# Kernel tuning notes

Measured on AMD Instinct MI355X. Metric: run time of the kernel, lower is better.

Reference implementation:

```python
import jax, jax.numpy as jnp
import numpy as np

TOP_K = 2


def setup_inputs() -> dict:
    key = jax.random.key(0)
    ks = jax.random.split(key, 5)
    B, N, C, FF, E = 2, 2048, 1024, 4096, 8
    x = jax.random.normal(ks[0], (B, N, C), dtype=jnp.float32)
    router_w = jax.random.normal(ks[1], (E, C), dtype=jnp.float32) * 0.02
    # xavier-uniform-like init for expert weights
    lim1 = np.sqrt(6.0 / (FF + C))
    expert_w1 = jax.random.uniform(ks[2], (E, FF, C), dtype=jnp.float32, minval=-lim1, maxval=lim1)
    expert_b1 = jnp.zeros((E, FF), dtype=jnp.float32)
    expert_w2 = jax.random.uniform(ks[3], (E, C, FF), dtype=jnp.float32, minval=-lim1, maxval=lim1)
    expert_b2 = jnp.zeros((E, C), dtype=jnp.float32)
    return {"x": x, "router_w": router_w, "expert_w1": expert_w1,
            "expert_b1": expert_b1, "expert_w2": expert_w2, "expert_b2": expert_b2}


def reference(x, router_w, expert_w1, expert_b1, expert_w2, expert_b2):
    # x: [B,N,C]; router_w: [E,C]; expert_w1: [E,FF,C]; expert_w2: [E,C,FF]
    router_logits = jnp.einsum('bnc,ec->bne', x, router_w)          # [B,N,E]
    router_probs = jax.nn.softmax(router_logits, axis=-1)
    expert_weights, expert_idx = jax.lax.top_k(router_probs, TOP_K)  # [B,N,K]
    expert_weights = expert_weights / (expert_weights.sum(axis=-1, keepdims=True) + 1e-9)
    # Dense all-expert FFN (avoids materializing per-token gathered weight matrices)
    h = jnp.einsum('bnc,efc->bnef', x, expert_w1) + expert_b1        # [B,N,E,FF]
    h = jax.nn.gelu(h, approximate=False)                            # torch nn.GELU = exact
    out_all = jnp.einsum('bnef,ecf->bnec', h, expert_w2) + expert_b2  # [B,N,E,C]
    # Gather top-k expert outputs and combine
    out_k = jnp.take_along_axis(out_all, expert_idx[..., None], axis=2)  # [B,N,K,C]
    return (out_k * expert_weights[..., None]).sum(axis=2)           # [B,N,C]
```

## Files before the change

### kernel.cpp

```cpp
#include <hip/hip_runtime.h>
#include <hip/hip_bf16.h>

#define TTOK  4096
#define CDIM  1024
#define FFDIM 4096
#define NEXP  8


typedef short short8 __attribute__((ext_vector_type(8)));
typedef float f32x4 __attribute__((ext_vector_type(4)));

__device__ __forceinline__ unsigned short f2bf(float f) {
    unsigned int u = __float_as_uint(f);
    u = u + 0x7fffu + ((u >> 16) & 1u);
    return (unsigned short)(u >> 16);
}

__global__ void cast_x_kernel(const float* __restrict__ x, unsigned short* __restrict__ xb) {
    int i = blockIdx.x * blockDim.x + threadIdx.x;
    float4 v = reinterpret_cast<const float4*>(x)[i];
    ushort4 o;
    o.x = f2bf(v.x); o.y = f2bf(v.y); o.z = f2bf(v.z); o.w = f2bf(v.w);
    reinterpret_cast<ushort4*>(xb)[i] = o;
}

__global__ void router_kernel(const float* __restrict__ x, const float* __restrict__ rw,
                              int* __restrict__ counts, int* __restrict__ btok,
                              float* __restrict__ bgate) {
    const int wave = threadIdx.x >> 6;
    const int lane = threadIdx.x & 63;
    const int t = blockIdx.x * 4 + wave;
    const float* xr = x + (size_t)t * CDIM;

    float acc[NEXP];
#pragma unroll
    for (int e = 0; e < NEXP; e++) acc[e] = 0.f;
    for (int c = lane; c < CDIM; c += 64) {
        float xv = xr[c];
#pragma unroll
        for (int e = 0; e < NEXP; e++) acc[e] += xv * rw[e * CDIM + c];
    }
#pragma unroll
    for (int e = 0; e < NEXP; e++) {
#pragma unroll
        for (int off = 32; off > 0; off >>= 1) acc[e] += __shfl_down(acc[e], off, 64);
    }
    if (lane == 0) {
        float mx = acc[0];
#pragma unroll
        for (int e = 1; e < NEXP; e++) mx = fmaxf(mx, acc[e]);
        float p[NEXP]; float s = 0.f;
#pragma unroll
        for (int e = 0; e < NEXP; e++) { p[e] = expf(acc[e] - mx); s += p[e]; }
        int i0 = 0;
#pragma unroll
        for (int e = 1; e < NEXP; e++) if (p[e] > p[i0]) i0 = e;
        int i1 = (i0 == 0) ? 1 : 0;
#pragma unroll
        for (int e = 0; e < NEXP; e++) if (e != i0 && p[e] > p[i1]) i1 = e;
        float pr0 = p[i0] / s, pr1 = p[i1] / s;
        float rs = 1.f / (pr0 + pr1 + 1e-9f);
        float w0 = pr0 * rs, w1 = pr1 * rs;
        int pos = atomicAdd(&counts[i0], 1);
        btok[i0 * TTOK + pos] = t; bgate[i0 * TTOK + pos] = w0;
        pos = atomicAdd(&counts[i1], 1);
        btok[i1 * TTOK + pos] = t; bgate[i1 * TTOK + pos] = w1;
    }
}

__global__ void offsets_kernel(const int* __restrict__ counts, int* __restrict__ offsets) {
    if (threadIdx.x == 0 && blockIdx.x == 0) {
        int s = 0;
        for (int e = 0; e < NEXP; e++) { offsets[e] = s; s += counts[e]; }
        offsets[NEXP] = s;
    }
}

__global__ __launch_bounds__(256) void gemm1_kernel(
    const unsigned short* __restrict__ xb, const float* __restrict__ w1,
    const float* __restrict__ b1, const int* __restrict__ counts,
    const int* __restrict__ offsets, const int* __restrict__ btok,
    unsigned short* __restrict__ H) {
    const int e = blockIdx.z;
    const int cnt = counts[e];
    const int m0 = blockIdx.y * 128;
    if (m0 >= cnt) return;
    const int n0 = blockIdx.x * 128;
    const int po = offsets[e];

    __shared__ unsigned short As[128][32];
    __shared__ unsigned short Bs[128][32];

    const int tid = threadIdx.x;
    const int wave = tid >> 6, lane = tid & 63;
    const int wm = (wave >> 1) << 6, wn = (wave & 1) << 6;
    const int lm = lane & 15, kq = lane >> 4;

    f32x4 acc[4][4];
#pragma unroll
    for (int i = 0; i < 4; i++)
#pragma unroll
        for (int j = 0; j < 4; j++) { f32x4 z = {0.f, 0.f, 0.f, 0.f}; acc[i][j] = z; }

    const float* w1e = w1 + (size_t)e * FFDIM * CDIM;
    const int arow = tid >> 1;
    const int acolb = (tid & 1) * 16;
    int tokA = -1;
    if (m0 + arow < cnt) tokA = btok[e * TTOK + m0 + arow];
    const int brow = tid >> 1;
    const int bcol = (tid & 1) * 16;

    for (int k0 = 0; k0 < CDIM; k0 += 32) {
        uint4 a0 = {0, 0, 0, 0}, a1 = {0, 0, 0, 0};
        if (tokA >= 0) {
            const uint4* src = reinterpret_cast<const uint4*>(xb + (size_t)tokA * CDIM + k0 + acolb);
            a0 = src[0]; a1 = src[1];
        }
        *reinterpret_cast<uint4*>(&As[arow][acolb]) = a0;
        *reinterpret_cast<uint4*>(&As[arow][acolb + 8]) = a1;
        {
            const float* src = w1e + (size_t)(n0 + brow) * CDIM + k0 + bcol;
            ushort4* dst = reinterpret_cast<ushort4*>(&Bs[brow][bcol]);
#pragma unroll
            for (int q = 0; q < 4; q++) {
                float4 v = reinterpret_cast<const float4*>(src)[q];
                ushort4 o; o.x = f2bf(v.x); o.y = f2bf(v.y); o.z = f2bf(v.z); o.w = f2bf(v.w);
                dst[q] = o;
            }
        }
        __syncthreads();
        short8 af[4], bfr[4];
#pragma unroll
        for (int i = 0; i < 4; i++) af[i] = *reinterpret_cast<const short8*>(&As[wm + i * 16 + lm][kq * 8]);
#pragma unroll
        for (int j = 0; j < 4; j++) bfr[j] = *reinterpret_cast<const short8*>(&Bs[wn + j * 16 + lm][kq * 8]);
#pragma unroll
        for (int i = 0; i < 4; i++)
#pragma unroll
            for (int j = 0; j < 4; j++)
                acc[i][j] = __builtin_amdgcn_mfma_f32_16x16x32_bf16(af[i], bfr[j], acc[i][j], 0, 0, 0);
        __syncthreads();
    }

#pragma unroll
    for (int j = 0; j < 4; j++) {
        const int fcol = n0 + wn + j * 16 + lm;
        const float bias = b1[e * FFDIM + fcol];
#pragma unroll
        for (int i = 0; i < 4; i++) {
#pragma unroll
            for (int r = 0; r < 4; r++) {
                const int mrow = m0 + wm + i * 16 + kq * 4 + r;
                if (mrow < cnt) {
                    float h = acc[i][j][r] + bias;
                    float g = 0.5f * h * (1.f + erff(h * 0.70710678118654752f));
                    H[(size_t)(po + mrow) * FFDIM + fcol] = f2bf(g);
                }
            }
        }
    }
}

__global__ __launch_bounds__(256) void gemm2_kernel(
    const unsigned short* __restrict__ H, const float* __restrict__ w2,
    const float* __restrict__ b2, const int* __restrict__ counts,
    const int* __restrict__ offsets, const int* __restrict__ btok,
    const float* __restrict__ bgate, float* __restrict__ out) {
    const int e = blockIdx.z;
    const int cnt = counts[e];
    const int m0 = blockIdx.y * 128;
    if (m0 >= cnt) return;
    const int n0 = blockIdx.x * 128;
    const int po = offsets[e];

    __shared__ unsigned short As[128][32];
    __shared__ unsigned short Bs[128][32];

    const int tid = threadIdx.x;
    const int wave = tid >> 6, lane = tid & 63;
    const int wm = (wave >> 1) << 6, wn = (wave & 1) << 6;
    const int lm = lane & 15, kq = lane >> 4;

    f32x4 acc[4][4];
#pragma unroll
    for (int i = 0; i < 4; i++)
#pragma unroll
        for (int j = 0; j < 4; j++) { f32x4 z = {0.f, 0.f, 0.f, 0.f}; acc[i][j] = z; }

    const float* w2e = w2 + (size_t)e * CDIM * FFDIM;
    const int arow = tid >> 1;
    const int acolb = (tid & 1) * 16;
    const bool aval = (m0 + arow < cnt);
    const unsigned short* asrc = H + (size_t)(po + m0 + arow) * FFDIM + acolb;
    const int brow = tid >> 1;
    const int bcol = (tid & 1) * 16;

    for (int k0 = 0; k0 < FFDIM; k0 += 32) {
        uint4 a0 = {0, 0, 0, 0}, a1 = {0, 0, 0, 0};
        if (aval) {
            const uint4* src = reinterpret_cast<const uint4*>(asrc + k0);
            a0 = src[0]; a1 = src[1];
        }
        *reinterpret_cast<uint4*>(&As[arow][acolb]) = a0;
        *reinterpret_cast<uint4*>(&As[arow][acolb + 8]) = a1;
        {
            const float* src = w2e + (size_t)(n0 + brow) * FFDIM + k0 + bcol;
            ushort4* dst = reinterpret_cast<ushort4*>(&Bs[brow][bcol]);
#pragma unroll
            for (int q = 0; q < 4; q++) {
                float4 v = reinterpret_cast<const float4*>(src)[q];
                ushort4 o; o.x = f2bf(v.x); o.y = f2bf(v.y); o.z = f2bf(v.z); o.w = f2bf(v.w);
                dst[q] = o;
            }
        }
        __syncthreads();
        short8 af[4], bfr[4];
#pragma unroll
        for (int i = 0; i < 4; i++) af[i] = *reinterpret_cast<const short8*>(&As[wm + i * 16 + lm][kq * 8]);
#pragma unroll
        for (int j = 0; j < 4; j++) bfr[j] = *reinterpret_cast<const short8*>(&Bs[wn + j * 16 + lm][kq * 8]);
#pragma unroll
        for (int i = 0; i < 4; i++)
#pragma unroll
            for (int j = 0; j < 4; j++)
                acc[i][j] = __builtin_amdgcn_mfma_f32_16x16x32_bf16(af[i], bfr[j], acc[i][j], 0, 0, 0);
        __syncthreads();
    }

    float bias[4];
#pragma unroll
    for (int j = 0; j < 4; j++) bias[j] = b2[e * CDIM + n0 + wn + j * 16 + lm];

#pragma unroll
    for (int i = 0; i < 4; i++) {
#pragma unroll
        for (int r = 0; r < 4; r++) {
            const int mrow = m0 + wm + i * 16 + kq * 4 + r;
            if (mrow < cnt) {
                const int tok = btok[e * TTOK + mrow];
                const float g = bgate[e * TTOK + mrow];
                float* orow = out + (size_t)tok * CDIM;
#pragma unroll
                for (int j = 0; j < 4; j++) {
                    const int c = n0 + wn + j * 16 + lm;
                    atomicAdd(orow + c, g * (acc[i][j][r] + bias[j]));
                }
            }
        }
    }
}

extern "C" void kernel_launch(void* const* d_in, const int* in_sizes, int n_in,
                              void* d_out, int out_size, void* d_ws, size_t ws_size,
                              hipStream_t stream) {
    const float* x  = (const float*)d_in[0];
    const float* rw = (const float*)d_in[1];
    const float* w1 = (const float*)d_in[2];
    const float* b1 = (const float*)d_in[3];
    const float* w2 = (const float*)d_in[4];
    const float* b2 = (const float*)d_in[5];
    float* out = (float*)d_out;

    char* ws = (char*)d_ws;
    int*   counts  = (int*)ws;
    int*   offsets = (int*)(ws + 64);
    int*   btok    = (int*)(ws + 4096);
    float* bgate   = (float*)(ws + 4096 + 131072);
    unsigned short* xb = (unsigned short*)(ws + (1u << 20));
    unsigned short* H  = (unsigned short*)(ws + (16u << 20));

    hipMemsetAsync(d_out, 0, (size_t)out_size * sizeof(float), stream);
    hipMemsetAsync(counts, 0, 64, stream);

    cast_x_kernel<<<(TTOK * CDIM) / (256 * 4), 256, 0, stream>>>(x, xb);
    router_kernel<<<TTOK / 4, 256, 0, stream>>>(x, rw, counts, btok, bgate);
    offsets_kernel<<<1, 64, 0, stream>>>(counts, offsets);
    gemm1_kernel<<<dim3(FFDIM / 128, TTOK / 128, NEXP), 256, 0, stream>>>(
        xb, w1, b1, counts, offsets, btok, H);
    gemm2_kernel<<<dim3(CDIM / 128, TTOK / 128, NEXP), 256, 0, stream>>>(
        H, w2, b2, counts, offsets, btok, bgate, out);
}
```

Before: 754.1 us.

## Pre-cast expert weights to bf16 and stream tiles via global_load_lds

When workspace is large enough, the expert weights are converted to bf16 in separate cast kernels before each GEMM. New GEMM kernels then load A/B tiles directly into LDS with global_load_lds instead of converting fp32 weights inside the loop. GEMM2 is also split along K into two halves so more blocks run, with partial results accumulated atomically. This adds full-weight cast passes each call and more atomics, and it depends on the workspace size to be selected.

```diff
diff --git a/kernel.cpp b/kernel.cpp
--- a/kernel.cpp
+++ b/kernel.cpp
@@ -1,5 +1,6 @@
 #include <hip/hip_runtime.h>
 #include <hip/hip_bf16.h>
+#include <cstdint>
 
 #define TTOK  4096
 #define CDIM  1024
@@ -16,12 +17,18 @@
     return (unsigned short)(u >> 16);
 }
 
-__global__ void cast_x_kernel(const float* __restrict__ x, unsigned short* __restrict__ xb) {
+__device__ __forceinline__ void gl_lds16(const unsigned short* g, unsigned short* l) {
+    __builtin_amdgcn_global_load_lds(
+        (const __attribute__((address_space(1))) unsigned int*)g,
+        (__attribute__((address_space(3))) unsigned int*)l, 16, 0, 0);
+}
+
+__global__ void cast_kernel(const float* __restrict__ src, unsigned short* __restrict__ dst) {
     int i = blockIdx.x * blockDim.x + threadIdx.x;
-    float4 v = reinterpret_cast<const float4*>(x)[i];
+    float4 v = reinterpret_cast<const float4*>(src)[i];
     ushort4 o;
     o.x = f2bf(v.x); o.y = f2bf(v.y); o.z = f2bf(v.z); o.w = f2bf(v.w);
-    reinterpret_cast<ushort4*>(xb)[i] = o;
+    reinterpret_cast<ushort4*>(dst)[i] = o;
 }
 
 __global__ void router_kernel(const float* __restrict__ x, const float* __restrict__ rw,
@@ -75,6 +82,179 @@
         offsets[NEXP] = s;
     }
 }
+
+
+__global__ __launch_bounds__(256) void gemm1f_kernel(
+    const unsigned short* __restrict__ xb, const unsigned short* __restrict__ w1b,
+    const float* __restrict__ b1, const int* __restrict__ counts,
+    const int* __restrict__ offsets, const int* __restrict__ btok,
+    unsigned short* __restrict__ H) {
+    const int e = blockIdx.z;
+    const int cnt = counts[e];
+    const int m0 = blockIdx.y * 128;
+    if (m0 >= cnt) return;
+    const int n0 = blockIdx.x * 128;
+    const int po = offsets[e];
+
+    __shared__ unsigned short As[128 * 32];
+    __shared__ unsigned short Bs[128 * 32];
+    __shared__ unsigned short Cs[64 * 128];
+
+    const int tid = threadIdx.x;
+    const int wave = tid >> 6, lane = tid & 63;
+    const int wm = (wave >> 1) << 6, wn = (wave & 1) << 6;
+    const int lm = lane & 15, kq = lane >> 4;
+
+    const int sr = tid >> 2;
+    const int sc = (tid & 3) << 3;
+    const int tA0 = btok[e * TTOK + min(m0 + sr, cnt - 1)];
+    const int tA1 = btok[e * TTOK + min(m0 + 64 + sr, cnt - 1)];
+    const unsigned short* ga0 = xb + (size_t)tA0 * CDIM + sc;
+    const unsigned short* ga1 = xb + (size_t)tA1 * CDIM + sc;
+    const unsigned short* gb0 = w1b + ((size_t)e * FFDIM + n0 + sr) * CDIM + sc;
+    const unsigned short* gb1 = gb0 + (size_t)64 * CDIM;
+    unsigned short* lA = &As[tid * 8];
+    unsigned short* lB = &Bs[tid * 8];
+
+    f32x4 acc[4][4];
+#pragma unroll
+    for (int i = 0; i < 4; i++)
+#pragma unroll
+        for (int j = 0; j < 4; j++) { f32x4 z = {0.f, 0.f, 0.f, 0.f}; acc[i][j] = z; }
+
+    for (int k0 = 0; k0 < CDIM; k0 += 32) {
+        gl_lds16(ga0 + k0, lA);
+        gl_lds16(ga1 + k0, lA + 64 * 32);
+        gl_lds16(gb0 + k0, lB);
+        gl_lds16(gb1 + k0, lB + 64 * 32);
+        __syncthreads();
+        short8 af[4], bfr[4];
+#pragma unroll
+        for (int i = 0; i < 4; i++) af[i] = *reinterpret_cast<const short8*>(&As[(wm + i * 16 + lm) * 32 + kq * 8]);
+#pragma unroll
+        for (int j = 0; j < 4; j++) bfr[j] = *reinterpret_cast<const short8*>(&Bs[(wn + j * 16 + lm) * 32 + kq * 8]);
+#pragma unroll
+        for (int i = 0; i < 4; i++)
+#pragma unroll
+            for (int j = 0; j < 4; j++)
+                acc[i][j] = __builtin_amdgcn_mfma_f32_16x16x32_bf16(af[i], bfr[j], acc[i][j], 0, 0, 0);
+        __syncthreads();
+    }
+
+    float bias[4];
+#pragma unroll
+    for (int j = 0; j < 4; j++) bias[j] = b1[e * FFDIM + n0 + wn + j * 16 + lm];
+
+#pragma unroll
+    for (int p = 0; p < 2; p++) {
+        if ((wave >> 1) == p) {
+#pragma unroll
+            for (int i = 0; i < 4; i++) {
+#pragma unroll
+                for (int r = 0; r < 4; r++) {
+                    const int row = i * 16 + kq * 4 + r;
+#pragma unroll
+                    for (int j = 0; j < 4; j++) {
+                        float h = acc[i][j][r] + bias[j];
+                        float g = 0.5f * h * (1.f + erff(h * 0.70710678118654752f));
+                        Cs[row * 128 + wn + j * 16 + lm] = f2bf(g);
+                    }
+                }
+            }
+        }
+        __syncthreads();
+#pragma unroll
+        for (int q = 0; q < 4; q++) {
+            const int c = q * 256 + tid;
+            const int row = c >> 4;
+            const int col8 = (c & 15) << 3;
+            const int mrow = m0 + p * 64 + row;
+            if (mrow < cnt)
+                *reinterpret_cast<uint4*>(&H[(size_t)(po + mrow) * FFDIM + n0 + col8]) =
+                    *reinterpret_cast<const uint4*>(&Cs[row * 128 + col8]);
+        }
+        __syncthreads();
+    }
+}
+
+__global__ __launch_bounds__(256) void gemm2f_kernel(
+    const unsigned short* __restrict__ H, const unsigned short* __restrict__ w2b,
+    const float* __restrict__ b2, const int* __restrict__ counts,
+    const int* __restrict__ offsets, const int* __restrict__ btok,
+    const float* __restrict__ bgate, float* __restrict__ out) {
+    const int e = blockIdx.z;
+    const int cnt = counts[e];
+    const int m0 = (blockIdx.y >> 1) * 128;
+    const int ks = blockIdx.y & 1;
+    if (m0 >= cnt) return;
+    const int n0 = blockIdx.x * 128;
+    const int po = offsets[e];
+
+    __shared__ unsigned short As[128 * 32];
+    __shared__ unsigned short Bs[128 * 32];
+
+    const int tid = threadIdx.x;
+    const int wave = tid >> 6, lane = tid & 63;
+    const int wm = (wave >> 1) << 6, wn = (wave & 1) << 6;
+    const int lm = lane & 15, kq = lane >> 4;
+
+    const int sr = tid >> 2;
+    const int sc = (tid & 3) << 3;
+    const int r0 = min(m0 + sr, cnt - 1);
+    const int r1 = min(m0 + 64 + sr, cnt - 1);
+    const unsigned short* ga0 = H + (size_t)(po + r0) * FFDIM + ks * 2048 + sc;
+    const unsigned short* ga1 = H + (size_t)(po + r1) * FFDIM + ks * 2048 + sc;
+    const unsigned short* gb0 = w2b + ((size_t)e * CDIM + n0 + sr) * FFDIM + ks * 2048 + sc;
+    const unsigned short* gb1 = gb0 + (size_t)64 * FFDIM;
+    unsigned short* lA = &As[tid * 8];
+    unsigned short* lB = &Bs[tid * 8];
+
+    f32x4 acc[4][4];
+#pragma unroll
+    for (int i = 0; i < 4; i++)
+#pragma unroll
+        for (int j = 0; j < 4; j++) { f32x4 z = {0.f, 0.f, 0.f, 0.f}; acc[i][j] = z; }
+
+    for (int k0 = 0; k0 < 2048; k0 += 32) {
+        gl_lds16(ga0 + k0, lA);
+        gl_lds16(ga1 + k0, lA + 64 * 32);
+        gl_lds16(gb0 + k0, lB);
+        gl_lds16(gb1 + k0, lB + 64 * 32);
+        __syncthreads();
+        short8 af[4], bfr[4];
+#pragma unroll
+        for (int i = 0; i < 4; i++) af[i] = *reinterpret_cast<const short8*>(&As[(wm + i * 16 + lm) * 32 + kq * 8]);
+#pragma unroll
+        for (int j = 0; j < 4; j++) bfr[j] = *reinterpret_cast<const short8*>(&Bs[(wn + j * 16 + lm) * 32 + kq * 8]);
+#pragma unroll
+        for (int i = 0; i < 4; i++)
+#pragma unroll
+            for (int j = 0; j < 4; j++)
+                acc[i][j] = __builtin_amdgcn_mfma_f32_16x16x32_bf16(af[i], bfr[j], acc[i][j], 0, 0, 0);
+        __syncthreads();
+    }
+
+    float bias[4];
+#pragma unroll
+    for (int j = 0; j < 4; j++) bias[j] = (ks == 0) ? b2[e * CDIM + n0 + wn + j * 16 + lm] : 0.f;
+
+#pragma unroll
+    for (int i = 0; i < 4; i++) {
+#pragma unroll
+        for (int r = 0; r < 4; r++) {
+            const int mrow = m0 + wm + i * 16 + kq * 4 + r;
+            if (mrow < cnt) {
+                const int tok = btok[e * TTOK + mrow];
+                const float g = bgate[e * TTOK + mrow];
+                float* orow = out + (size_t)tok * CDIM;
+#pragma unroll
+                for (int j = 0; j < 4; j++)
+                    atomicAdd(orow + n0 + wn + j * 16 + lm, g * (acc[i][j][r] + bias[j]));
+            }
+        }
+    }
+}
+
 
 __global__ __launch_bounds__(256) void gemm1_kernel(
     const unsigned short* __restrict__ xb, const float* __restrict__ w1,
@@ -266,17 +446,36 @@
     int*   offsets = (int*)(ws + 64);
     int*   btok    = (int*)(ws + 4096);
     float* bgate   = (float*)(ws + 4096 + 131072);
-    unsigned short* xb = (unsigned short*)(ws + (1u << 20));
-    unsigned short* H  = (unsigned short*)(ws + (16u << 20));
 
     hipMemsetAsync(d_out, 0, (size_t)out_size * sizeof(float), stream);
     hipMemsetAsync(counts, 0, 64, stream);
 
-    cast_x_kernel<<<(TTOK * CDIM) / (256 * 4), 256, 0, stream>>>(x, xb);
-    router_kernel<<<TTOK / 4, 256, 0, stream>>>(x, rw, counts, btok, bgate);
-    offsets_kernel<<<1, 64, 0, stream>>>(counts, offsets);
-    gemm1_kernel<<<dim3(FFDIM / 128, TTOK / 128, NEXP), 256, 0, stream>>>(
-        xb, w1, b1, counts, offsets, btok, H);
-    gemm2_kernel<<<dim3(CDIM / 128, TTOK / 128, NEXP), 256, 0, stream>>>(
-        H, w2, b2, counts, offsets, btok, bgate, out);
-}
+    const bool fast = ws_size >= ((size_t)137 << 20);
+
+    if (fast) {
+        unsigned short* xb = (unsigned short*)(ws + ((size_t)1 << 20));
+        unsigned short* Wb = (unsigned short*)(ws + ((size_t)9 << 20));
+        unsigned short* H  = (unsigned short*)(ws + ((size_t)73 << 20));
+
+        cast_kernel<<<(TTOK * CDIM) / (256 * 4), 256, 0, stream>>>(x, xb);
+        router_kernel<<<TTOK / 4, 256, 0, stream>>>(x, rw, counts, btok, bgate);
+        offsets_kernel<<<1, 64, 0, stream>>>(counts, offsets);
+        cast_kernel<<<(NEXP * FFDIM * CDIM) / (256 * 4), 256, 0, stream>>>(w1, Wb);
+        gemm1f_kernel<<<dim3(FFDIM / 128, TTOK / 128, NEXP), 256, 0, stream>>>(
+            xb, Wb, b1, counts, offsets, btok, H);
+        cast_kernel<<<(NEXP * CDIM * FFDIM) / (256 * 4), 256, 0, stream>>>(w2, Wb);
+        gemm2f_kernel<<<dim3(CDIM / 128, (TTOK / 128) * 2, NEXP), 256, 0, stream>>>(
+            H, Wb, b2, counts, offsets, btok, bgate, out);
+    } else {
+        unsigned short* xb = (unsigned short*)(ws + ((size_t)1 << 20));
+        unsigned short* H  = (unsigned short*)(ws + ((size_t)16 << 20));
+
+        cast_kernel<<<(TTOK * CDIM) / (256 * 4), 256, 0, stream>>>(x, xb);
+        router_kernel<<<TTOK / 4, 256, 0, stream>>>(x, rw, counts, btok, bgate);
+        offsets_kernel<<<1, 64, 0, stream>>>(counts, offsets);
+        gemm1_kernel<<<dim3(FFDIM / 128, TTOK / 128, NEXP), 256, 0, stream>>>(
+            xb, w1, b1, counts, offsets, btok, H);
+        gemm2_kernel<<<dim3(CDIM / 128, TTOK / 128, NEXP), 256, 0, stream>>>(
+            H, w2, b2, counts, offsets, btok, bgate, out);
+    }
+}
```

Measured after the change: 708.4 us. 1.06x faster.
